# Optimization experiments

Hardware: AMD Instinct MI355X
Metric: run time of the kernel (lower is better)

## Reference

```python
import jax, jax.numpy as jnp
import numpy as np

N = 50000
E = 800000
D_IN = 256
D_OUT = 256
ALPHA = 0.5


def setup_inputs() -> dict:
    key = jax.random.key(0)
    k1, k2, k3, k4, k5, k6 = jax.random.split(key, 6)
    stdv = 1.0 / np.sqrt(D_OUT)
    return {
        "input": jax.random.normal(k1, (N, D_IN), dtype=jnp.float32),
        "adj_src": jax.random.randint(k2, (E,), 0, N, dtype=jnp.int64),
        "adj_dst": jax.random.randint(k3, (E,), 0, N, dtype=jnp.int64),
        "adj_w": jax.random.uniform(k4, (E,), dtype=jnp.float32),
        "init_input": jax.random.normal(k5, (N, D_OUT), dtype=jnp.float32),
        "weight": jax.random.uniform(k6, (D_IN, D_OUT), dtype=jnp.float32,
                                     minval=-stdv, maxval=stdv),
    }


def reference(input, adj_src, adj_dst, adj_w, init_input, weight):
    # support = input @ W          [N, D_OUT] (dense GEMM)
    support = jnp.matmul(input, weight)
    # spmm: out[dst] += w * support[src]   (COO aggregate)
    msgs = support[adj_src] * adj_w[:, None]          # [E, D_OUT]
    agg = jax.ops.segment_sum(msgs, adj_dst, num_segments=N)  # [N, D_OUT]
    # alpha-blended residual + ReLU (bias=False, act=ReLU)
    out = agg * ALPHA + init_input * (1.0 - ALPHA)
    return jax.nn.relu(out)
```

## Files before the change

kernel.cpp:

```cpp
#include <hip/hip_runtime.h>
#include <hip/hip_fp16.h>

#define ALPHA 0.5f

typedef short short8v __attribute__((ext_vector_type(8)));
typedef float f32x4 __attribute__((ext_vector_type(4)));

__device__ __forceinline__ unsigned short f2bf(float f) {
  union { float f; unsigned u; } v; v.f = f;
  unsigned r = v.u + 0x7FFFu + ((v.u >> 16) & 1u);
  return (unsigned short)(r >> 16);
}
__device__ __forceinline__ float bf2f(unsigned short u) {
  union { unsigned u; float f; } v; v.u = ((unsigned)u) << 16;
  return v.f;
}

__global__ void transpose_w(const float* __restrict__ W, unsigned short* __restrict__ Wt) {
  __shared__ float tile[16][17];
  int kb = blockIdx.x * 16, nb = blockIdx.y * 16;
  tile[threadIdx.y][threadIdx.x] = W[(kb + threadIdx.y) * 256 + nb + threadIdx.x];
  __syncthreads();
  Wt[(nb + threadIdx.y) * 256 + kb + threadIdx.x] = f2bf(tile[threadIdx.x][threadIdx.y]);
}

__global__ void cvt_input(const float* __restrict__ A, unsigned short* __restrict__ Ab, int n8) {
  int i = blockIdx.x * blockDim.x + threadIdx.x;
  int stride = gridDim.x * blockDim.x;
  for (; i < n8; i += stride) {
    float4 a = *reinterpret_cast<const float4*>(&A[i * 8]);
    float4 b = *reinterpret_cast<const float4*>(&A[i * 8 + 4]);
    unsigned short o[8] = {f2bf(a.x), f2bf(a.y), f2bf(a.z), f2bf(a.w),
                           f2bf(b.x), f2bf(b.y), f2bf(b.z), f2bf(b.w)};
    *reinterpret_cast<short8v*>(&Ab[i * 8]) = *reinterpret_cast<short8v*>(o);
  }
}

__global__ __launch_bounds__(256) void gemm_mfma(
    const unsigned short* __restrict__ Ab, const unsigned short* __restrict__ Wt,
    unsigned short* __restrict__ C, int M) {
  __shared__ char smem[2][24576];
  const int tid = threadIdx.x;
  const int lane = tid & 63;
  const int w = tid >> 6;
  const int wm = w >> 1, wn = w & 1;
  const int row0 = blockIdx.x * 128;

  f32x4 acc[4][8];
  #pragma unroll
  for (int m = 0; m < 4; ++m)
    #pragma unroll
    for (int n = 0; n < 8; ++n) acc[m][n] = (f32x4){0.f, 0.f, 0.f, 0.f};

  int arow[2];
  #pragma unroll
  for (int i = 0; i < 2; ++i) {
    int r = row0 + (w * 2 + i) * 16 + (lane & 15);
    arow[i] = (r < M) ? r : (M - 1);
  }
  const int kh = (lane >> 4) * 8;

  int cur = 0;
  {
    #pragma unroll
    for (int i = 0; i < 2; ++i) {
      int s = w * 2 + i;
      const unsigned short* g = Ab + (size_t)arow[i] * 256 + kh;
      __builtin_amdgcn_global_load_lds(
          (const __attribute__((address_space(1))) void*)g,
          (__attribute__((address_space(3))) void*)(&smem[0][s * 1024]),
          16, 0, 0);
    }
    #pragma unroll
    for (int i = 0; i < 4; ++i) {
      int s = w * 4 + i;
      const unsigned short* g = Wt + (size_t)(s * 16 + (lane & 15)) * 256 + kh;
      __builtin_amdgcn_global_load_lds(
          (const __attribute__((address_space(1))) void*)g,
          (__attribute__((address_space(3))) void*)(&smem[0][8192 + s * 1024]),
          16, 0, 0);
    }
    __syncthreads();
  }

  #pragma unroll
  for (int t = 0; t < 8; ++t) {
    const bool pf = (t < 7);
    if (pf) {
      const int k0 = (t + 1) * 32;
      #pragma unroll
      for (int i = 0; i < 2; ++i) {
        int s = w * 2 + i;
        const unsigned short* g = Ab + (size_t)arow[i] * 256 + k0 + kh;
        __builtin_amdgcn_global_load_lds(
            (const __attribute__((address_space(1))) void*)g,
            (__attribute__((address_space(3))) void*)(&smem[cur ^ 1][s * 1024]),
            16, 0, 0);
      }
      #pragma unroll
      for (int i = 0; i < 4; ++i) {
        int s = w * 4 + i;
        const unsigned short* g = Wt + (size_t)(s * 16 + (lane & 15)) * 256 + k0 + kh;
        __builtin_amdgcn_global_load_lds(
            (const __attribute__((address_space(1))) void*)g,
            (__attribute__((address_space(3))) void*)(&smem[cur ^ 1][8192 + s * 1024]),
            16, 0, 0);
      }
    }
    short8v af[4], bfv[8];
    #pragma unroll
    for (int m = 0; m < 4; ++m)
      af[m] = *reinterpret_cast<const short8v*>(&smem[cur][(wm * 4 + m) * 1024 + lane * 16]);
    #pragma unroll
    for (int n = 0; n < 8; ++n)
      bfv[n] = *reinterpret_cast<const short8v*>(&smem[cur][8192 + (wn * 8 + n) * 1024 + lane * 16]);
    #pragma unroll
    for (int m = 0; m < 4; ++m)
      #pragma unroll
      for (int n = 0; n < 8; ++n)
        acc[m][n] = __builtin_amdgcn_mfma_f32_16x16x32_bf16(af[m], bfv[n], acc[m][n], 0, 0, 0);
    __syncthreads();
    cur ^= 1;
  }

  #pragma unroll
  for (int m = 0; m < 4; ++m) {
    #pragma unroll
    for (int n = 0; n < 8; ++n) {
      const int col = wn * 128 + n * 16 + (lane & 15);
      #pragma unroll
      for (int r = 0; r < 4; ++r) {
        const int row = row0 + wm * 64 + m * 16 + (lane >> 4) * 4 + r;
        if (row < M) C[(size_t)row * 256 + col] = f2bf(acc[m][n][r]);
      }
    }
  }
}

__global__ void histogram_dst(const int* __restrict__ dst, int* __restrict__ deg, int E) {
  int i = blockIdx.x * blockDim.x + threadIdx.x;
  if (i < E) atomicAdd(&deg[dst[i]], 1);
}

__global__ __launch_bounds__(256) void scan_pass1(const int* __restrict__ deg,
                                                  int* __restrict__ excl,
                                                  int* __restrict__ partial, int N) {
  const int tid = threadIdx.x;
  const int base = blockIdx.x * 1024 + tid * 4;
  int4 v = make_int4(0, 0, 0, 0);
  if (base + 3 < N) v = *reinterpret_cast<const int4*>(&deg[base]);
  else {
    if (base + 0 < N) v.x = deg[base + 0];
    if (base + 1 < N) v.y = deg[base + 1];
    if (base + 2 < N) v.z = deg[base + 2];
  }
  const int s = v.x + v.y + v.z + v.w;
  const int lane = tid & 63, wid = tid >> 6;
  int ps = s;
  #pragma unroll
  for (int off = 1; off < 64; off <<= 1) {
    int t = __shfl_up(ps, off, 64);
    if (lane >= off) ps += t;
  }
  __shared__ int wsum[4];
  if (lane == 63) wsum[wid] = ps;
  __syncthreads();
  int woff = 0;
  #pragma unroll
  for (int w2 = 0; w2 < 4; ++w2) woff += (w2 < wid) ? wsum[w2] : 0;
  const int texcl = woff + ps - s;
  int4 e = make_int4(texcl, texcl + v.x, texcl + v.x + v.y, texcl + v.x + v.y + v.z);
  if (base + 3 < N) *reinterpret_cast<int4*>(&excl[base]) = e;
  else {
    if (base + 0 < N) excl[base + 0] = e.x;
    if (base + 1 < N) excl[base + 1] = e.y;
    if (base + 2 < N) excl[base + 2] = e.z;
  }
  if (tid == 255) partial[blockIdx.x] = woff + ps;
}

__global__ __launch_bounds__(256) void scan_pass2(const int* __restrict__ excl,
                                                  const int* __restrict__ partial,
                                                  int* __restrict__ row_ptr,
                                                  int* __restrict__ cursor, int N, int NB) {
  __shared__ int s_off;
  const int tid = threadIdx.x;
  if (tid < 64) {
    int v = (tid < NB && tid < (int)blockIdx.x) ? partial[tid] : 0;
    #pragma unroll
    for (int off = 1; off < 64; off <<= 1) v += __shfl_xor(v, off, 64);
    if (tid == 0) s_off = v;
  }
  __syncthreads();
  const int off = s_off;
  const int base = blockIdx.x * 1024 + tid * 4;
  if (base + 3 < N) {
    int4 v = *reinterpret_cast<const int4*>(&excl[base]);
    v.x += off; v.y += off; v.z += off; v.w += off;
    *reinterpret_cast<int4*>(&row_ptr[base]) = v;
    *reinterpret_cast<int4*>(&cursor[base]) = v;
  } else {
    for (int j = 0; j < 4; ++j)
      if (base + j < N) { int v = excl[base + j] + off; row_ptr[base + j] = v; cursor[base + j] = v; }
  }
}

__global__ void reindex_edges(const int* __restrict__ src, const int* __restrict__ dst,
                              const float* __restrict__ w, int* __restrict__ cursor,
                              unsigned* __restrict__ edges, int E) {
  int i = blockIdx.x * blockDim.x + threadIdx.x;
  if (i < E) {
    int d = dst[i];
    int slot = atomicAdd(&cursor[d], 1);
    unsigned hb = __half_as_ushort(__float2half(w[i] * ALPHA));
    edges[slot] = ((unsigned)src[i] << 15) | (hb >> 1);
  }
}

__device__ __forceinline__ float unpack_w(unsigned p) {
  return __half2float(__ushort_as_half((unsigned short)((p & 0x7FFFu) << 1)));
}

__global__ __launch_bounds__(256) void aggregate(
    const unsigned short* __restrict__ support,
    const int* __restrict__ row_ptr, const int* __restrict__ deg,
    const unsigned* __restrict__ edges,
    const float* __restrict__ init, float* __restrict__ out, int N) {
  int node = blockIdx.x * 4 + (threadIdx.x >> 6);
  if (node >= N) return;
  int lane = threadIdx.x & 63;
  int start = row_ptr[node], cnt = deg[node];

  float4 ini = *reinterpret_cast<const float4*>(&init[(size_t)node * 256 + lane * 4]);

  float4 acc = make_float4(0.f, 0.f, 0.f, 0.f);
  int e = 0;
  for (; e + 7 < cnt; e += 8) {
    unsigned p[8];
    #pragma unroll
    for (int j = 0; j < 8; ++j) p[j] = edges[start + e + j];
    ushort4 v[8];
    #pragma unroll
    for (int j = 0; j < 8; ++j)
      v[j] = *reinterpret_cast<const ushort4*>(&support[(size_t)(p[j] >> 15) * 256 + lane * 4]);
    #pragma unroll
    for (int j = 0; j < 8; ++j) {
      float wj = unpack_w(p[j]);
      acc.x += wj * bf2f(v[j].x);
      acc.y += wj * bf2f(v[j].y);
      acc.z += wj * bf2f(v[j].z);
      acc.w += wj * bf2f(v[j].w);
    }
  }
  for (; e < cnt; ++e) {
    unsigned p = edges[start + e];
    ushort4 v = *reinterpret_cast<const ushort4*>(&support[(size_t)(p >> 15) * 256 + lane * 4]);
    float wj = unpack_w(p);
    acc.x += wj * bf2f(v.x); acc.y += wj * bf2f(v.y);
    acc.z += wj * bf2f(v.z); acc.w += wj * bf2f(v.w);
  }
  float4 o;
  o.x = fmaxf(acc.x + (1.f - ALPHA) * ini.x, 0.f);
  o.y = fmaxf(acc.y + (1.f - ALPHA) * ini.y, 0.f);
  o.z = fmaxf(acc.z + (1.f - ALPHA) * ini.z, 0.f);
  o.w = fmaxf(acc.w + (1.f - ALPHA) * ini.w, 0.f);
  *reinterpret_cast<float4*>(&out[(size_t)node * 256 + lane * 4]) = o;
}

extern "C" void kernel_launch(void* const* d_in, const int* in_sizes, int n_in,
                              void* d_out, int out_size, void* d_ws, size_t ws_size,
                              hipStream_t stream) {
  const float* input   = (const float*)d_in[0];
  const int*   adj_src = (const int*)d_in[1];
  const int*   adj_dst = (const int*)d_in[2];
  const float* adj_w   = (const float*)d_in[3];
  const float* init_in = (const float*)d_in[4];
  const float* weight  = (const float*)d_in[5];
  float* out = (float*)d_out;

  const int N = in_sizes[0] / 256;
  const int E = in_sizes[1];

  char* ws = (char*)d_ws;
  unsigned short* support = (unsigned short*)ws; ws += (size_t)N * 256 * 2;
  unsigned short* Ab      = (unsigned short*)ws; ws += (size_t)N * 256 * 2;
  unsigned short* Wt      = (unsigned short*)ws; ws += 256 * 256 * 2;
  int* deg     = (int*)ws; ws += (size_t)N * 4;
  int* row_ptr = (int*)ws; ws += (size_t)N * 4;
  int* cursor  = (int*)ws; ws += (size_t)N * 4;
  int* excl    = (int*)ws; ws += (size_t)N * 4;
  int* partial = (int*)ws; ws += 256;
  unsigned* edges = (unsigned*)ws; ws += (size_t)E * 4;

  const int NB = (N + 1023) / 1024;

  transpose_w<<<dim3(16, 16), dim3(16, 16), 0, stream>>>(weight, Wt);
  cvt_input<<<2048, 256, 0, stream>>>(input, Ab, N * 256 / 8);
  gemm_mfma<<<dim3((N + 127) / 128), 256, 0, stream>>>(Ab, Wt, support, N);

  hipMemsetAsync(deg, 0, (size_t)N * 4, stream);
  histogram_dst<<<(E + 255) / 256, 256, 0, stream>>>(adj_dst, deg, E);
  scan_pass1<<<NB, 256, 0, stream>>>(deg, excl, partial, N);
  scan_pass2<<<NB, 256, 0, stream>>>(excl, partial, row_ptr, cursor, N, NB);
  reindex_edges<<<(E + 255) / 256, 256, 0, stream>>>(adj_src, adj_dst, adj_w, cursor, edges, E);

  aggregate<<<(N + 3) / 4, 256, 0, stream>>>(support, row_ptr, deg, edges, init_in, out, N);
}
```

Before: 199.3 us.

## Fuse prep kernels, shrink GEMM tile, vectorize edge kernels, use row_ptr end

Merges the weight transpose, input bf16 conversion and degree zeroing into one prep kernel, removing two launches and a memset. Halves the GEMM row tile to 64 so each block uses less LDS and fewer accumulators, giving more blocks and higher occupancy at the cost of reloading W more often. Histogram and reindex now process four edges per thread with vector loads. Aggregate reads degree from row_ptr[node+1]-row_ptr[node] instead of a separate deg array.

```diff
diff --git a/kernel.cpp b/kernel.cpp
--- a/kernel.cpp
+++ b/kernel.cpp
@@ -16,68 +16,66 @@
   return v.f;
 }
 
-__global__ void transpose_w(const float* __restrict__ W, unsigned short* __restrict__ Wt) {
-  __shared__ float tile[16][17];
-  int kb = blockIdx.x * 16, nb = blockIdx.y * 16;
-  tile[threadIdx.y][threadIdx.x] = W[(kb + threadIdx.y) * 256 + nb + threadIdx.x];
-  __syncthreads();
-  Wt[(nb + threadIdx.y) * 256 + kb + threadIdx.x] = f2bf(tile[threadIdx.x][threadIdx.y]);
-}
-
-__global__ void cvt_input(const float* __restrict__ A, unsigned short* __restrict__ Ab, int n8) {
-  int i = blockIdx.x * blockDim.x + threadIdx.x;
-  int stride = gridDim.x * blockDim.x;
-  for (; i < n8; i += stride) {
-    float4 a = *reinterpret_cast<const float4*>(&A[i * 8]);
-    float4 b = *reinterpret_cast<const float4*>(&A[i * 8 + 4]);
-    unsigned short o[8] = {f2bf(a.x), f2bf(a.y), f2bf(a.z), f2bf(a.w),
-                           f2bf(b.x), f2bf(b.y), f2bf(b.z), f2bf(b.w)};
-    *reinterpret_cast<short8v*>(&Ab[i * 8]) = *reinterpret_cast<short8v*>(o);
+__global__ __launch_bounds__(256) void prep(
+    const float* __restrict__ W, unsigned short* __restrict__ Wt,
+    const float* __restrict__ A, unsigned short* __restrict__ Ab,
+    int* __restrict__ deg, int n8, int N) {
+  const int tid = threadIdx.x;
+  if (blockIdx.x < 256) {
+    __shared__ float tile[16][17];
+    const int bx = blockIdx.x;
+    const int kb = (bx & 15) * 16, nb = (bx >> 4) * 16;
+    const int tx = tid & 15, ty = tid >> 4;
+    tile[ty][tx] = W[(kb + ty) * 256 + nb + tx];
+    __syncthreads();
+    Wt[(nb + ty) * 256 + kb + tx] = f2bf(tile[tx][ty]);
+  } else {
+    const int base = (blockIdx.x - 256) * 256 + tid;
+    const int stride = (gridDim.x - 256) * 256;
+    if (base < N) deg[base] = 0;
+    for (int i = base; i < n8; i += stride) {
+      float4 a = *reinterpret_cast<const float4*>(&A[i * 8]);
+      float4 b = *reinterpret_cast<const float4*>(&A[i * 8 + 4]);
+      unsigned short o[8] = {f2bf(a.x), f2bf(a.y), f2bf(a.z), f2bf(a.w),
+                             f2bf(b.x), f2bf(b.y), f2bf(b.z), f2bf(b.w)};
+      *reinterpret_cast<short8v*>(&Ab[i * 8]) = *reinterpret_cast<short8v*>(o);
+    }
   }
 }
 
 __global__ __launch_bounds__(256) void gemm_mfma(
     const unsigned short* __restrict__ Ab, const unsigned short* __restrict__ Wt,
     unsigned short* __restrict__ C, int M) {
-  __shared__ char smem[2][24576];
+  __shared__ char smem[2][20480];
   const int tid = threadIdx.x;
   const int lane = tid & 63;
   const int w = tid >> 6;
-  const int wm = w >> 1, wn = w & 1;
-  const int row0 = blockIdx.x * 128;
-
-  f32x4 acc[4][8];
+  const int row0 = blockIdx.x * 64;
+
+  f32x4 acc[4][4];
   #pragma unroll
   for (int m = 0; m < 4; ++m)
     #pragma unroll
-    for (int n = 0; n < 8; ++n) acc[m][n] = (f32x4){0.f, 0.f, 0.f, 0.f};
-
-  int arow[2];
-  #pragma unroll
-  for (int i = 0; i < 2; ++i) {
-    int r = row0 + (w * 2 + i) * 16 + (lane & 15);
-    arow[i] = (r < M) ? r : (M - 1);
-  }
+    for (int n = 0; n < 4; ++n) acc[m][n] = (f32x4){0.f, 0.f, 0.f, 0.f};
+
+  int r = row0 + w * 16 + (lane & 15);
+  const int arow = (r < M) ? r : (M - 1);
   const int kh = (lane >> 4) * 8;
 
   int cur = 0;
   {
-    #pragma unroll
-    for (int i = 0; i < 2; ++i) {
-      int s = w * 2 + i;
-      const unsigned short* g = Ab + (size_t)arow[i] * 256 + kh;
-      __builtin_amdgcn_global_load_lds(
-          (const __attribute__((address_space(1))) void*)g,
-          (__attribute__((address_space(3))) void*)(&smem[0][s * 1024]),
-          16, 0, 0);
-    }
+    const unsigned short* ga = Ab + (size_t)arow * 256 + kh;
+    __builtin_amdgcn_global_load_lds(
+        (const __attribute__((address_space(1))) void*)ga,
+        (__attribute__((address_space(3))) void*)(&smem[0][w * 1024]),
+        16, 0, 0);
     #pragma unroll
     for (int i = 0; i < 4; ++i) {
       int s = w * 4 + i;
       const unsigned short* g = Wt + (size_t)(s * 16 + (lane & 15)) * 256 + kh;
       __builtin_amdgcn_global_load_lds(
           (const __attribute__((address_space(1))) void*)g,
-          (__attribute__((address_space(3))) void*)(&smem[0][8192 + s * 1024]),
+          (__attribute__((address_space(3))) void*)(&smem[0][4096 + s * 1024]),
           16, 0, 0);
     }
     __syncthreads();
@@ -88,36 +86,32 @@
     const bool pf = (t < 7);
     if (pf) {
       const int k0 = (t + 1) * 32;
-      #pragma unroll
-      for (int i = 0; i < 2; ++i) {
-        int s = w * 2 + i;
-        const unsigned short* g = Ab + (size_t)arow[i] * 256 + k0 + kh;
-        __builtin_amdgcn_global_load_lds(
-            (const __attribute__((address_space(1))) void*)g,
-            (__attribute__((address_space(3))) void*)(&smem[cur ^ 1][s * 1024]),
-            16, 0, 0);
-      }
+      const unsigned short* ga = Ab + (size_t)arow * 256 + k0 + kh;
+      __builtin_amdgcn_global_load_lds(
+          (const __attribute__((address_space(1))) void*)ga,
+          (__attribute__((address_space(3))) void*)(&smem[cur ^ 1][w * 1024]),
+          16, 0, 0);
       #pragma unroll
       for (int i = 0; i < 4; ++i) {
         int s = w * 4 + i;
         const unsigned short* g = Wt + (size_t)(s * 16 + (lane & 15)) * 256 + k0 + kh;
         __builtin_amdgcn_global_load_lds(
             (const __attribute__((address_space(1))) void*)g,
-            (__attribute__((address_space(3))) void*)(&smem[cur ^ 1][8192 + s * 1024]),
+            (__attribute__((address_space(3))) void*)(&smem[cur ^ 1][4096 + s * 1024]),
             16, 0, 0);
       }
     }
-    short8v af[4], bfv[8];
+    short8v af[4], bfv[4];
     #pragma unroll
     for (int m = 0; m < 4; ++m)
-      af[m] = *reinterpret_cast<const short8v*>(&smem[cur][(wm * 4 + m) * 1024 + lane * 16]);
-    #pragma unroll
-    for (int n = 0; n < 8; ++n)
-      bfv[n] = *reinterpret_cast<const short8v*>(&smem[cur][8192 + (wn * 8 + n) * 1024 + lane * 16]);
+      af[m] = *reinterpret_cast<const short8v*>(&smem[cur][m * 1024 + lane * 16]);
+    #pragma unroll
+    for (int n = 0; n < 4; ++n)
+      bfv[n] = *reinterpret_cast<const short8v*>(&smem[cur][4096 + (w * 4 + n) * 1024 + lane * 16]);
     #pragma unroll
     for (int m = 0; m < 4; ++m)
       #pragma unroll
-      for (int n = 0; n < 8; ++n)
+      for (int n = 0; n < 4; ++n)
         acc[m][n] = __builtin_amdgcn_mfma_f32_16x16x32_bf16(af[m], bfv[n], acc[m][n], 0, 0, 0);
     __syncthreads();
     cur ^= 1;
@@ -126,20 +120,27 @@
   #pragma unroll
   for (int m = 0; m < 4; ++m) {
     #pragma unroll
-    for (int n = 0; n < 8; ++n) {
-      const int col = wn * 128 + n * 16 + (lane & 15);
+    for (int n = 0; n < 4; ++n) {
+      const int col = w * 64 + n * 16 + (lane & 15);
       #pragma unroll
-      for (int r = 0; r < 4; ++r) {
-        const int row = row0 + wm * 64 + m * 16 + (lane >> 4) * 4 + r;
-        if (row < M) C[(size_t)row * 256 + col] = f2bf(acc[m][n][r]);
+      for (int r2 = 0; r2 < 4; ++r2) {
+        const int row = row0 + m * 16 + (lane >> 4) * 4 + r2;
+        if (row < M) C[(size_t)row * 256 + col] = f2bf(acc[m][n][r2]);
       }
     }
   }
 }
 
-__global__ void histogram_dst(const int* __restrict__ dst, int* __restrict__ deg, int E) {
-  int i = blockIdx.x * blockDim.x + threadIdx.x;
-  if (i < E) atomicAdd(&deg[dst[i]], 1);
+__global__ __launch_bounds__(256) void histogram_dst(const int* __restrict__ dst,
+                                                     int* __restrict__ deg, int E) {
+  int i = (blockIdx.x * blockDim.x + threadIdx.x) * 4;
+  if (i + 3 < E) {
+    int4 d = *reinterpret_cast<const int4*>(&dst[i]);
+    atomicAdd(&deg[d.x], 1); atomicAdd(&deg[d.y], 1);
+    atomicAdd(&deg[d.z], 1); atomicAdd(&deg[d.w], 1);
+  } else {
+    for (; i < E; ++i) atomicAdd(&deg[dst[i]], 1);
+  }
 }
 
 __global__ __launch_bounds__(256) void scan_pass1(const int* __restrict__ deg,
@@ -182,7 +183,8 @@
 __global__ __launch_bounds__(256) void scan_pass2(const int* __restrict__ excl,
                                                   const int* __restrict__ partial,
                                                   int* __restrict__ row_ptr,
-                                                  int* __restrict__ cursor, int N, int NB) {
+                                                  int* __restrict__ cursor,
+                                                  int N, int NB, int E) {
   __shared__ int s_off;
   const int tid = threadIdx.x;
   if (tid < 64) {
@@ -191,6 +193,7 @@
     for (int off = 1; off < 64; off <<= 1) v += __shfl_xor(v, off, 64);
     if (tid == 0) s_off = v;
   }
+  if (blockIdx.x == 0 && tid == 0) row_ptr[N] = E;
   __syncthreads();
   const int off = s_off;
   const int base = blockIdx.x * 1024 + tid * 4;
@@ -205,15 +208,30 @@
   }
 }
 
-__global__ void reindex_edges(const int* __restrict__ src, const int* __restrict__ dst,
-                              const float* __restrict__ w, int* __restrict__ cursor,
-                              unsigned* __restrict__ edges, int E) {
-  int i = blockIdx.x * blockDim.x + threadIdx.x;
-  if (i < E) {
-    int d = dst[i];
-    int slot = atomicAdd(&cursor[d], 1);
-    unsigned hb = __half_as_ushort(__float2half(w[i] * ALPHA));
-    edges[slot] = ((unsigned)src[i] << 15) | (hb >> 1);
+__global__ __launch_bounds__(256) void reindex_edges(
+    const int* __restrict__ src, const int* __restrict__ dst,
+    const float* __restrict__ w, int* __restrict__ cursor,
+    unsigned* __restrict__ edges, int E) {
+  int i = (blockIdx.x * blockDim.x + threadIdx.x) * 4;
+  if (i + 3 < E) {
+    int4 sv = *reinterpret_cast<const int4*>(&src[i]);
+    int4 dv = *reinterpret_cast<const int4*>(&dst[i]);
+    float4 wv = *reinterpret_cast<const float4*>(&w[i]);
+    int s_[4] = {sv.x, sv.y, sv.z, sv.w};
+    int d_[4] = {dv.x, dv.y, dv.z, dv.w};
+    float w_[4] = {wv.x, wv.y, wv.z, wv.w};
+    #pragma unroll
+    for (int j = 0; j < 4; ++j) {
+      int slot = atomicAdd(&cursor[d_[j]], 1);
+      unsigned hb = __half_as_ushort(__float2half(w_[j] * ALPHA));
+      edges[slot] = ((unsigned)s_[j] << 15) | (hb >> 1);
+    }
+  } else {
+    for (; i < E; ++i) {
+      int slot = atomicAdd(&cursor[dst[i]], 1);
+      unsigned hb = __half_as_ushort(__float2half(w[i] * ALPHA));
+      edges[slot] = ((unsigned)src[i] << 15) | (hb >> 1);
+    }
   }
 }
 
@@ -223,13 +241,14 @@
 
 __global__ __launch_bounds__(256) void aggregate(
     const unsigned short* __restrict__ support,
-    const int* __restrict__ row_ptr, const int* __restrict__ deg,
+    const int* __restrict__ row_ptr,
     const unsigned* __restrict__ edges,
     const float* __restrict__ init, float* __restrict__ out, int N) {
   int node = blockIdx.x * 4 + (threadIdx.x >> 6);
   if (node >= N) return;
   int lane = threadIdx.x & 63;
-  int start = row_ptr[node], cnt = deg[node];
+  int start = row_ptr[node];
+  int cnt = row_ptr[node + 1] - start;
 
   float4 ini = *reinterpret_cast<const float4*>(&init[(size_t)node * 256 + lane * 4]);
 
@@ -286,7 +305,7 @@
   unsigned short* Ab      = (unsigned short*)ws; ws += (size_t)N * 256 * 2;
   unsigned short* Wt      = (unsigned short*)ws; ws += 256 * 256 * 2;
   int* deg     = (int*)ws; ws += (size_t)N * 4;
-  int* row_ptr = (int*)ws; ws += (size_t)N * 4;
+  int* row_ptr = (int*)ws; ws += (size_t)(N + 1) * 4;
   int* cursor  = (int*)ws; ws += (size_t)N * 4;
   int* excl    = (int*)ws; ws += (size_t)N * 4;
   int* partial = (int*)ws; ws += 256;
@@ -294,15 +313,13 @@
 
   const int NB = (N + 1023) / 1024;
 
-  transpose_w<<<dim3(16, 16), dim3(16, 16), 0, stream>>>(weight, Wt);
-  cvt_input<<<2048, 256, 0, stream>>>(input, Ab, N * 256 / 8);
-  gemm_mfma<<<dim3((N + 127) / 128), 256, 0, stream>>>(Ab, Wt, support, N);
-
-  hipMemsetAsync(deg, 0, (size_t)N * 4, stream);
-  histogram_dst<<<(E + 255) / 256, 256, 0, stream>>>(adj_dst, deg, E);
+  prep<<<2048, 256, 0, stream>>>(weight, Wt, input, Ab, deg, N * 256 / 8, N);
+  gemm_mfma<<<(N + 63) / 64, 256, 0, stream>>>(Ab, Wt, support, N);
+
+  histogram_dst<<<(E / 4 + 255) / 256, 256, 0, stream>>>(adj_dst, deg, E);
   scan_pass1<<<NB, 256, 0, stream>>>(deg, excl, partial, N);
-  scan_pass2<<<NB, 256, 0, stream>>>(excl, partial, row_ptr, cursor, N, NB);
-  reindex_edges<<<(E + 255) / 256, 256, 0, stream>>>(adj_src, adj_dst, adj_w, cursor, edges, E);
-
-  aggregate<<<(N + 3) / 4, 256, 0, stream>>>(support, row_ptr, deg, edges, init_in, out, N);
-}
+  scan_pass2<<<NB, 256, 0, stream>>>(excl, partial, row_ptr, cursor, N, NB, E);
+  reindex_edges<<<(E / 4 + 255) / 256, 256, 0, stream>>>(adj_src, adj_dst, adj_w, cursor, edges, E);
+
+  aggregate<<<(N + 3) / 4, 256, 0, stream>>>(support, row_ptr, edges, init_in, out, N);
+}
```

Result: no change. 202.3 us (+1.5%).
